# Kernel optimization log

Measured on AMD Instinct MI355X. Metric: run time of the kernel, lower is better.

The kernel has to match this reference:

```python
import jax, jax.numpy as jnp
import numpy as np

B, L, D, H = 2, 2048, 2048, 16
DH = D // H
ROPE_BASE = 10000.0


def _rope_cos_sin(seq_len, d_head, dtype=jnp.float32):
    # half-split RoPE: frequencies over even indices, repeated for both halves
    inv_freq = 1.0 / (ROPE_BASE ** (jnp.arange(0, d_head, 2, dtype=jnp.float32) / d_head))
    freqs = jnp.arange(seq_len, dtype=jnp.float32)[:, None] * inv_freq[None, :]  # [L, DH/2]
    emb = jnp.concatenate([freqs, freqs], axis=-1)  # [L, DH]
    return jnp.cos(emb).astype(dtype), jnp.sin(emb).astype(dtype)


def _rotate_half(x):
    x1, x2 = jnp.split(x, 2, axis=-1)
    return jnp.concatenate([-x2, x1], axis=-1)


def _apply_rope(x, cos, sin):
    # x: [B, H, L, DH]; cos/sin: [L, DH]
    return x * cos[None, None, :, :] + _rotate_half(x) * sin[None, None, :, :]


def setup_inputs() -> dict:
    key = jax.random.key(0)
    k1, k2, k3 = jax.random.split(key, 3)
    x = jax.random.normal(k1, (B, L, D), dtype=jnp.float32)
    w_qkv = jax.random.normal(k2, (3 * D, D), dtype=jnp.float32) * 0.02
    w_out = jax.random.normal(k3, (D, D), dtype=jnp.float32) * 0.02
    return {"x": x, "w_qkv": w_qkv, "w_out": w_out}


def reference(x, w_qkv, w_out):
    b, l, d = x.shape
    dh = d // H
    qkv = jnp.einsum('bld,ed->ble', x, w_qkv)  # [B, L, 3D]
    qkv = qkv.reshape(b, l, 3, H, dh)
    q = jnp.transpose(qkv[:, :, 0], (0, 2, 1, 3))  # [B, H, L, DH]
    k = jnp.transpose(qkv[:, :, 1], (0, 2, 1, 3))
    v = jnp.transpose(qkv[:, :, 2], (0, 2, 1, 3))
    cos, sin = _rope_cos_sin(l, dh, x.dtype)
    q = _apply_rope(q, cos, sin)
    k = _apply_rope(k, cos, sin)
    scale = 1.0 / jnp.sqrt(jnp.asarray(dh, dtype=x.dtype))
    scores = jnp.einsum('bhqd,bhkd->bhqk', q, k) * scale  # [B, H, L, L]
    causal = jnp.tril(jnp.ones((l, l), dtype=bool))
    scores = jnp.where(causal[None, None], scores, jnp.asarray(-jnp.inf, dtype=scores.dtype))
    attn = jax.nn.softmax(scores, axis=-1)
    out = jnp.einsum('bhqk,bhkd->bhqd', attn, v)  # [B, H, L, DH]
    out = jnp.transpose(out, (0, 2, 1, 3)).reshape(b, l, d)
    return jnp.einsum('bld,ed->ble', out, w_out)
```

## Files before the change

kernel.cpp:

```cpp
#include <hip/hip_runtime.h>
#include <hip/hip_bf16.h>

#define B_  2
#define L_  2048
#define D_  2048
#define H_  16
#define DH_ 128

typedef __attribute__((ext_vector_type(8))) short bf16x8;
typedef __attribute__((ext_vector_type(4))) short short4v;
typedef __attribute__((ext_vector_type(4))) float f32x4;
typedef __attribute__((ext_vector_type(16))) float f32x16;

__device__ __forceinline__ short f2bf(float f) {
  unsigned u = __float_as_uint(f);
  u = u + 0x7fffu + ((u >> 16) & 1u);
  return (short)(u >> 16);
}
__device__ __forceinline__ float bf2f(short s) {
  return __uint_as_float(((unsigned)(unsigned short)s) << 16);
}
__device__ __forceinline__ int pkbf(float a, float b) {
  return (int)(unsigned short)f2bf(a) | (((int)(unsigned short)f2bf(b)) << 16);
}

__global__ __launch_bounds__(256) void cvt_bf16_kernel(
    const float* __restrict__ in, short* __restrict__ out, int n4) {
  int i = blockIdx.x * 256 + threadIdx.x;
  if (i >= n4) return;
  float4 v = ((const float4*)in)[i];
  short4v o;
  o[0] = f2bf(v.x); o[1] = f2bf(v.y); o[2] = f2bf(v.z); o[3] = f2bf(v.w);
  ((short4v*)out)[i] = o;
}

__global__ __launch_bounds__(256) void rope_table_kernel(
    float* __restrict__ cost, float* __restrict__ sint) {
  int idx = blockIdx.x * 256 + threadIdx.x;
  int l = idx >> 6, j = idx & 63;
  float inv = powf(10000.0f, -(float)(2 * j) * (1.0f / 128.0f));
  float ang = (float)l * inv;
  cost[idx] = cosf(ang);
  sint[idx] = sinf(ang);
}

template<bool BF16OUT>
__global__ __launch_bounds__(256) void gemm_bt_kernel(
    const short* __restrict__ A, const short* __restrict__ Bm,
    void* __restrict__ Cv, int M, int N, int K) {
  __shared__ short As[128 * 32];
  __shared__ short Bs[128 * 32];
  const int tm = blockIdx.x * 128;
  const int tn = blockIdx.y * 128;
  const int tid = threadIdx.x;
  const int w = tid >> 6, l = tid & 63;
  const int wm = (w >> 1) * 64, wn = (w & 1) * 64;
  const int lr = l & 15, lk = (l >> 4) * 8;

  f32x4 acc[4][4] = {};

  for (int k0 = 0; k0 < K; k0 += 32) {
#pragma unroll
    for (int c = 0; c < 2; ++c) {
      int chunk = w * 2 + c;
      int elem = chunk * 512 + l * 8;
      int row = elem >> 5, col = elem & 31;
      __builtin_amdgcn_global_load_lds(
          (const __attribute__((address_space(1))) void*)(A + (size_t)(tm + row) * K + k0 + col),
          (__attribute__((address_space(3))) void*)(As + chunk * 512), 16, 0, 0);
      __builtin_amdgcn_global_load_lds(
          (const __attribute__((address_space(1))) void*)(Bm + (size_t)(tn + row) * K + k0 + col),
          (__attribute__((address_space(3))) void*)(Bs + chunk * 512), 16, 0, 0);
    }
    __syncthreads();
    bf16x8 af[4], bfr[4];
#pragma unroll
    for (int i = 0; i < 4; ++i) af[i]  = *(const bf16x8*)&As[(wm + i * 16 + lr) * 32 + lk];
#pragma unroll
    for (int j = 0; j < 4; ++j) bfr[j] = *(const bf16x8*)&Bs[(wn + j * 16 + lr) * 32 + lk];
#pragma unroll
    for (int i = 0; i < 4; ++i)
#pragma unroll
      for (int j = 0; j < 4; ++j)
        acc[i][j] = __builtin_amdgcn_mfma_f32_16x16x32_bf16(af[i], bfr[j], acc[i][j], 0, 0, 0);
    __syncthreads();
  }

  const int r0 = (l >> 4) * 4;
#pragma unroll
  for (int i = 0; i < 4; ++i)
#pragma unroll
    for (int j = 0; j < 4; ++j)
#pragma unroll
      for (int r = 0; r < 4; ++r) {
        size_t idx = (size_t)(tm + wm + i * 16 + r0 + r) * N + (tn + wn + j * 16 + lr);
        if (BF16OUT) ((short*)Cv)[idx] = f2bf(acc[i][j][r]);
        else         ((float*)Cv)[idx] = acc[i][j][r];
      }
}

__global__ __launch_bounds__(256) void rope_pack_kernel(
    const short* __restrict__ qkv, const float* __restrict__ cost,
    const float* __restrict__ sint, short* __restrict__ Qp,
    short* __restrict__ Kp) {
  int idx = blockIdx.x * 256 + threadIdx.x;
  int dh = idx & 63;
  int h  = (idx >> 6) & 15;
  int l  = (idx >> 10) & 2047;
  int b  = idx >> 21;
  size_t src = (size_t)(b * L_ + l) * (3 * D_);
  int e = h * DH_ + dh;
  float c = cost[l * 64 + dh], s = sint[l * 64 + dh];
  float q1 = bf2f(qkv[src + e]),        q2 = bf2f(qkv[src + e + 64]);
  float k1 = bf2f(qkv[src + D_ + e]),   k2 = bf2f(qkv[src + D_ + e + 64]);
  const float scale = 0.08838834764831845f;
  size_t dst = ((size_t)(b * H_ + h) * L_ + l) * DH_ + dh;
  Qp[dst]      = f2bf((q1 * c - q2 * s) * scale);
  Qp[dst + 64] = f2bf((q2 * c + q1 * s) * scale);
  Kp[dst]      = f2bf(k1 * c - k2 * s);
  Kp[dst + 64] = f2bf(k2 * c + k1 * s);
}

__global__ __launch_bounds__(256) void transpose_v_kernel(
    const short* __restrict__ qkv, short* __restrict__ VtG) {
  __shared__ short T[64 * 64];
  int bid = blockIdx.x;
  int lt = bid & 31, dt = (bid >> 5) & 1, bh = bid >> 6;
  int b = bh >> 4, h = bh & 15;
  int l0 = lt * 64, d0 = dt * 64;
  int tid = threadIdx.x;
#pragma unroll
  for (int it = 0; it < 2; ++it) {
    int row = it * 32 + (tid >> 3);
    int c   = (tid & 7) * 8;
    bf16x8 v = *(const bf16x8*)&qkv[(size_t)(b * L_ + l0 + row) * (3 * D_) + 2 * D_ + h * DH_ + d0 + c];
#pragma unroll
    for (int jj = 0; jj < 8; ++jj)
      T[row * 64 + ((c + jj + row) & 63)] = v[jj];
  }
  __syncthreads();
  int d = tid >> 2, lc = (tid & 3) * 16;
  short tmp[16];
#pragma unroll
  for (int j = 0; j < 16; ++j)
    tmp[j] = T[(lc + j) * 64 + ((d + lc + j) & 63)];
  size_t obase = (size_t)(bh * DH_ + d0 + d) * L_ + l0 + lc;
  *(bf16x8*)&VtG[obase]     = *(bf16x8*)&tmp[0];
  *(bf16x8*)&VtG[obase + 8] = *(bf16x8*)&tmp[8];
}

__global__ __launch_bounds__(256) void attn_kernel(
    const short* __restrict__ Qp, const short* __restrict__ Kp,
    const short* __restrict__ VtG, short* __restrict__ Out) {
  __shared__ short lds[2][16384];

  const int f   = blockIdx.x;
  const int bh  = (f & 7) + 8 * (f >> 7);
  const int qt  = (f >> 3) & 15;
  const int q0  = qt * 128;
  const int tid = threadIdx.x;
  const int w = tid >> 6, l = tid & 63;
  const int lq = l & 31, hi = l >> 5;
  const int qw = q0 + w * 32;
  const int b = bh >> 4, h = bh & 15;
  const size_t kqbase = (size_t)bh * (L_ * DH_);

  bf16x8 qf[8];
#pragma unroll
  for (int st = 0; st < 8; ++st)
    qf[st] = *(const bf16x8*)&Qp[kqbase + (size_t)(qw + lq) * DH_ + st * 16 + hi * 8];

  f32x16 oacc[4];
#pragma unroll
  for (int dm = 0; dm < 4; ++dm)
#pragma unroll
    for (int r = 0; r < 16; ++r) oacc[dm][r] = 0.f;
  float m_run = -1e30f, l_run = 0.f;

  const int nt = qt * 2 + 2;

  auto stage = [&](int bf, int kt) {
    int k0 = kt * 64;
#pragma unroll
    for (int i = 0; i < 4; ++i) {
      int c = w * 4 + i;
      int X = c * 1024 + l * 16;
      {
        int row = X >> 8, bcol = (X & 255) ^ ((row & 7) << 4);
        __builtin_amdgcn_global_load_lds(
            (const __attribute__((address_space(1))) void*)(Kp + kqbase + (size_t)(k0 + row) * DH_ + (bcol >> 1)),
            (__attribute__((address_space(3))) void*)(&lds[bf][c * 512]), 16, 0, 0);
      }
      {
        int row = X >> 7, bcol = (X & 127) ^ ((row & 7) << 4);
        __builtin_amdgcn_global_load_lds(
            (const __attribute__((address_space(1))) void*)(VtG + (size_t)(bh * DH_ + row) * L_ + k0 + (bcol >> 1)),
            (__attribute__((address_space(3))) void*)(&lds[bf][8192 + c * 512]), 16, 0, 0);
      }
    }
  };

  auto compute = [&](int bf, int kt) {
    int k0 = kt * 64;
    if (k0 > qw + 31) return;
    const char* ksB = (const char*)&lds[bf][0];
    const char* vsB = (const char*)&lds[bf][8192];

    f32x16 sacc[2];
#pragma unroll
    for (int fm = 0; fm < 2; ++fm)
#pragma unroll
      for (int r = 0; r < 16; ++r) sacc[fm][r] = 0.f;
#pragma unroll
    for (int st = 0; st < 8; ++st) {
#pragma unroll
      for (int fm = 0; fm < 2; ++fm) {
        int krow = fm * 32 + lq;
        int byte = (krow << 8) + ((st * 32 + hi * 16) ^ ((krow & 7) << 4));
        bf16x8 kf = *(const bf16x8*)(ksB + byte);
        sacc[fm] = __builtin_amdgcn_mfma_f32_32x32x16_bf16(kf, qf[st], sacc[fm], 0, 0, 0);
      }
    }

    if (k0 + 63 > qw) {
      int q = qw + lq;
#pragma unroll
      for (int fm = 0; fm < 2; ++fm)
#pragma unroll
        for (int r = 0; r < 16; ++r) {
          int k = k0 + fm * 32 + (r & 3) + 8 * (r >> 2) + 4 * hi;
          if (k > q) sacc[fm][r] = -1e30f;
        }
    }

    float pmax = sacc[0][0];
#pragma unroll
    for (int fm = 0; fm < 2; ++fm)
#pragma unroll
      for (int r = 0; r < 16; ++r) pmax = fmaxf(pmax, sacc[fm][r]);
    pmax = fmaxf(pmax, __shfl_xor(pmax, 32));
    float mnew = fmaxf(m_run, pmax);
    float alpha = __expf(m_run - mnew);
    m_run = mnew;
    float rsum = 0.f;
#pragma unroll
    for (int fm = 0; fm < 2; ++fm)
#pragma unroll
      for (int r = 0; r < 16; ++r) {
        float e = __expf(sacc[fm][r] - mnew);
        sacc[fm][r] = e;
        rsum += e;
      }
    rsum += __shfl_xor(rsum, 32);
    l_run = l_run * alpha + rsum;
#pragma unroll
    for (int dm = 0; dm < 4; ++dm)
#pragma unroll
      for (int r = 0; r < 16; ++r) oacc[dm][r] *= alpha;

    int pb[16];
#pragma unroll
    for (int fm = 0; fm < 2; ++fm)
#pragma unroll
      for (int i2 = 0; i2 < 8; ++i2)
        pb[fm * 8 + i2] = pkbf(sacc[fm][2 * i2], sacc[fm][2 * i2 + 1]);

#pragma unroll
    for (int kk = 0; kk < 4; ++kk) {
      int idx0 = (kk >> 1) * 8 + (kk & 1) * 4;
      int sw0 = __shfl_xor(pb[idx0],     32);
      int sw1 = __shfl_xor(pb[idx0 + 1], 32);
      int sw2 = __shfl_xor(pb[idx0 + 2], 32);
      int sw3 = __shfl_xor(pb[idx0 + 3], 32);
      union { int i[4]; bf16x8 v; } u;
      u.i[0] = hi ? sw2 : pb[idx0];
      u.i[1] = hi ? sw3 : pb[idx0 + 1];
      u.i[2] = hi ? pb[idx0 + 2] : sw0;
      u.i[3] = hi ? pb[idx0 + 3] : sw1;
#pragma unroll
      for (int dm = 0; dm < 4; ++dm) {
        int vrow = dm * 32 + lq;
        int byte = (vrow << 7) + ((kk * 32 + hi * 16) ^ ((vrow & 7) << 4));
        bf16x8 vf = *(const bf16x8*)(vsB + byte);
        oacc[dm] = __builtin_amdgcn_mfma_f32_32x32x16_bf16(vf, u.v, oacc[dm], 0, 0, 0);
      }
    }
  };

  stage(0, 0);
  __syncthreads();
  for (int kt = 0; kt < nt; ++kt) {
    if (kt + 1 < nt) stage((kt + 1) & 1, kt + 1);
    compute(kt & 1, kt);
    __syncthreads();
  }

  float inv = 1.0f / l_run;
  int q = qw + lq;
  size_t rowbase = ((size_t)(b * L_ + q)) * D_ + h * DH_;
#pragma unroll
  for (int dm = 0; dm < 4; ++dm)
#pragma unroll
    for (int g = 0; g < 4; ++g) {
      short4v s4;
#pragma unroll
      for (int t = 0; t < 4; ++t) s4[t] = f2bf(oacc[dm][4 * g + t] * inv);
      *(short4v*)&Out[rowbase + dm * 32 + 8 * g + 4 * hi] = s4;
    }
}

extern "C" void kernel_launch(void* const* d_in, const int* in_sizes, int n_in,
                              void* d_out, int out_size, void* d_ws, size_t ws_size,
                              hipStream_t stream) {
  const float* x     = (const float*)d_in[0];
  const float* w_qkv = (const float*)d_in[1];
  const float* w_out = (const float*)d_in[2];
  float* out = (float*)d_out;

  char* ws = (char*)d_ws;
  size_t off = 0;
  auto alloc = [&](size_t bytes) -> char* {
    char* p = ws + off;
    off += (bytes + 255) & ~(size_t)255;
    return p;
  };
  const size_t nX = (size_t)B_ * L_ * D_;
  const size_t nWqkv = (size_t)3 * D_ * D_;
  const size_t nWout = (size_t)D_ * D_;
  short* xb    = (short*)alloc(nX * 2);
  short* wqkvb = (short*)alloc(nWqkv * 2);
  short* woutb = (short*)alloc(nWout * 2);
  short* qkvb  = (short*)alloc((size_t)B_ * L_ * 3 * D_ * 2);
  short* Qp    = (short*)alloc(nX * 2);
  short* Kp    = (short*)alloc(nX * 2);
  short* VtG   = (short*)alloc(nX * 2);
  short* attnb = (short*)alloc(nX * 2);
  float* cost  = (float*)alloc((size_t)L_ * 64 * 4);
  float* sint  = (float*)alloc((size_t)L_ * 64 * 4);

  cvt_bf16_kernel<<<(int)(nX / 1024), 256, 0, stream>>>(x, xb, (int)(nX / 4));
  cvt_bf16_kernel<<<(int)(nWqkv / 1024), 256, 0, stream>>>(w_qkv, wqkvb, (int)(nWqkv / 4));
  cvt_bf16_kernel<<<(int)(nWout / 1024), 256, 0, stream>>>(w_out, woutb, (int)(nWout / 4));
  rope_table_kernel<<<(L_ * 64) / 256, 256, 0, stream>>>(cost, sint);
  gemm_bt_kernel<true><<<dim3(32, 48), 256, 0, stream>>>(xb, wqkvb, (void*)qkvb,
                                                         B_ * L_, 3 * D_, D_);
  rope_pack_kernel<<<(int)(nX / 512), 256, 0, stream>>>(qkvb, cost, sint, Qp, Kp);
  transpose_v_kernel<<<2048, 256, 0, stream>>>(qkvb, VtG);
  attn_kernel<<<512, 256, 0, stream>>>(Qp, Kp, VtG, attnb);
  gemm_bt_kernel<false><<<dim3(32, 16), 256, 0, stream>>>(attnb, woutb, (void*)out,
                                                          B_ * L_, D_, D_);
}
```

Before: 448.5 us.

## Rewrite GEMM with 256x128 tiles, triple-buffered LDS, swizzle and block remap

Replaces the 128x128 single-buffered GEMM with a 512-thread kernel computing 256x128 tiles over K-steps of 64. Global-to-LDS loads run through a three-stage ring buffer, prefetching two tiles ahead and waiting with explicit vmcnt counts, so memory latency overlaps the MFMA work. LDS rows use an XOR swizzle to avoid bank conflicts, and block IDs are remapped for better L2 locality. MFMA sections are wrapped in raised wave priority. The costs are 144KB of LDS per block, which limits occupancy, and more fragile hand-written synchronisation.

New measurement: 395.9 us. -11.7%, faster.

```diff
diff --git a/kernel.cpp b/kernel.cpp
--- a/kernel.cpp
+++ b/kernel.cpp
@@ -45,57 +45,128 @@
 }
 
 template<bool BF16OUT>
-__global__ __launch_bounds__(256) void gemm_bt_kernel(
+__global__ __launch_bounds__(512, 2) void gemm256_kernel(
     const short* __restrict__ A, const short* __restrict__ Bm,
-    void* __restrict__ Cv, int M, int N, int K) {
-  __shared__ short As[128 * 32];
-  __shared__ short Bs[128 * 32];
-  const int tm = blockIdx.x * 128;
-  const int tn = blockIdx.y * 128;
+    void* __restrict__ Cv, int M, int N, int K, int nbn) {
+  __shared__ short lds[3][24576];
+  const int NT = K >> 6;
   const int tid = threadIdx.x;
   const int w = tid >> 6, l = tid & 63;
-  const int wm = (w >> 1) * 64, wn = (w & 1) * 64;
-  const int lr = l & 15, lk = (l >> 4) * 8;
+  const int wrm = w >> 1, wnn = w & 1;
+  const int lr = l & 15, c4 = l >> 4;
+
+  const int cpx = gridDim.x >> 3;
+  const int bid = blockIdx.x;
+  const int swz = (bid & 7) * cpx + (bid >> 3);
+  const int bm = swz / nbn, bn = swz % nbn;
+  const int tm = bm * 256, tn = bn * 128;
+
+  const char* srcA[4];
+  const char* srcB[2];
+#pragma unroll
+  for (int s = 0; s < 4; ++s) {
+    int X = (s * 512 + tid) * 16;
+    int row = X >> 7;
+    int koff = (X & 127) ^ ((row & 7) << 4);
+    srcA[s] = (const char*)A + ((size_t)(tm + row) * K) * 2 + koff;
+  }
+#pragma unroll
+  for (int s = 0; s < 2; ++s) {
+    int X = (s * 512 + tid) * 16;
+    int row = X >> 7;
+    int koff = (X & 127) ^ ((row & 7) << 4);
+    srcB[s] = (const char*)Bm + ((size_t)(tn + row) * K) * 2 + koff;
+  }
+
+  int offA[4][2], offB[4][2];
+#pragma unroll
+  for (int m = 0; m < 4; ++m) {
+    int row = wrm * 64 + m * 16 + lr;
+#pragma unroll
+    for (int kk = 0; kk < 2; ++kk)
+      offA[m][kk] = row * 128 + ((kk * 64 + c4 * 16) ^ ((row & 7) << 4));
+  }
+#pragma unroll
+  for (int n = 0; n < 4; ++n) {
+    int row = wnn * 64 + n * 16 + lr;
+#pragma unroll
+    for (int kk = 0; kk < 2; ++kk)
+      offB[n][kk] = row * 128 + ((kk * 64 + c4 * 16) ^ ((row & 7) << 4));
+  }
+
+  auto issueA = [&](int jj, int buf) {
+#pragma unroll
+    for (int s = 0; s < 4; ++s)
+      __builtin_amdgcn_global_load_lds(
+          (const __attribute__((address_space(1))) void*)(srcA[s] + (size_t)jj * 128),
+          (__attribute__((address_space(3))) void*)(&lds[buf][s * 4096 + w * 512]),
+          16, 0, 0);
+  };
+  auto issueB = [&](int jj, int buf) {
+#pragma unroll
+    for (int s = 0; s < 2; ++s)
+      __builtin_amdgcn_global_load_lds(
+          (const __attribute__((address_space(1))) void*)(srcB[s] + (size_t)jj * 128),
+          (__attribute__((address_space(3))) void*)(&lds[buf][16384 + s * 4096 + w * 512]),
+          16, 0, 0);
+  };
 
   f32x4 acc[4][4] = {};
 
-  for (int k0 = 0; k0 < K; k0 += 32) {
-#pragma unroll
-    for (int c = 0; c < 2; ++c) {
-      int chunk = w * 2 + c;
-      int elem = chunk * 512 + l * 8;
-      int row = elem >> 5, col = elem & 31;
-      __builtin_amdgcn_global_load_lds(
-          (const __attribute__((address_space(1))) void*)(A + (size_t)(tm + row) * K + k0 + col),
-          (__attribute__((address_space(3))) void*)(As + chunk * 512), 16, 0, 0);
-      __builtin_amdgcn_global_load_lds(
-          (const __attribute__((address_space(1))) void*)(Bm + (size_t)(tn + row) * K + k0 + col),
-          (__attribute__((address_space(3))) void*)(Bs + chunk * 512), 16, 0, 0);
-    }
-    __syncthreads();
-    bf16x8 af[4], bfr[4];
-#pragma unroll
-    for (int i = 0; i < 4; ++i) af[i]  = *(const bf16x8*)&As[(wm + i * 16 + lr) * 32 + lk];
-#pragma unroll
-    for (int j = 0; j < 4; ++j) bfr[j] = *(const bf16x8*)&Bs[(wn + j * 16 + lr) * 32 + lk];
-#pragma unroll
-    for (int i = 0; i < 4; ++i)
-#pragma unroll
-      for (int j = 0; j < 4; ++j)
-        acc[i][j] = __builtin_amdgcn_mfma_f32_16x16x32_bf16(af[i], bfr[j], acc[i][j], 0, 0, 0);
-    __syncthreads();
-  }
-
-  const int r0 = (l >> 4) * 4;
-#pragma unroll
-  for (int i = 0; i < 4; ++i)
-#pragma unroll
-    for (int j = 0; j < 4; ++j)
+  issueA(0, 0); issueB(0, 0);
+  if (NT > 1) { issueA(1, 1); issueB(1, 1); }
+
+  int cur = 0;
+  for (int j = 0; j < NT; ++j) {
+    if (j == NT - 1) asm volatile("s_waitcnt vmcnt(0)" ::: "memory");
+    else             asm volatile("s_waitcnt vmcnt(6)" ::: "memory");
+    __builtin_amdgcn_s_barrier();
+    int pf = cur + 2; if (pf >= 3) pf -= 3;
+    const char* aB = (const char*)&lds[cur][0];
+    const char* bB = (const char*)&lds[cur][16384];
+
+    if (j + 2 < NT) issueA(j + 2, pf);
+    bf16x8 af[4], bfv[4];
+#pragma unroll
+    for (int m = 0; m < 4; ++m) af[m]  = *(const bf16x8*)(aB + offA[m][0]);
+#pragma unroll
+    for (int n = 0; n < 4; ++n) bfv[n] = *(const bf16x8*)(bB + offB[n][0]);
+    __builtin_amdgcn_s_barrier();
+    __builtin_amdgcn_s_setprio(1);
+#pragma unroll
+    for (int m = 0; m < 4; ++m)
+#pragma unroll
+      for (int n = 0; n < 4; ++n)
+        acc[m][n] = __builtin_amdgcn_mfma_f32_16x16x32_bf16(af[m], bfv[n], acc[m][n], 0, 0, 0);
+    __builtin_amdgcn_s_setprio(0);
+
+    if (j + 2 < NT) issueB(j + 2, pf);
+#pragma unroll
+    for (int m = 0; m < 4; ++m) af[m]  = *(const bf16x8*)(aB + offA[m][1]);
+#pragma unroll
+    for (int n = 0; n < 4; ++n) bfv[n] = *(const bf16x8*)(bB + offB[n][1]);
+    __builtin_amdgcn_s_barrier();
+    __builtin_amdgcn_s_setprio(1);
+#pragma unroll
+    for (int m = 0; m < 4; ++m)
+#pragma unroll
+      for (int n = 0; n < 4; ++n)
+        acc[m][n] = __builtin_amdgcn_mfma_f32_16x16x32_bf16(af[m], bfv[n], acc[m][n], 0, 0, 0);
+    __builtin_amdgcn_s_setprio(0);
+
+    cur = cur + 1; if (cur >= 3) cur = 0;
+  }
+
+#pragma unroll
+  for (int m = 0; m < 4; ++m)
+#pragma unroll
+    for (int n = 0; n < 4; ++n)
 #pragma unroll
       for (int r = 0; r < 4; ++r) {
-        size_t idx = (size_t)(tm + wm + i * 16 + r0 + r) * N + (tn + wn + j * 16 + lr);
-        if (BF16OUT) ((short*)Cv)[idx] = f2bf(acc[i][j][r]);
-        else         ((float*)Cv)[idx] = acc[i][j][r];
+        size_t idx = (size_t)(tm + wrm * 64 + m * 16 + c4 * 4 + r) * N
+                   + (tn + wnn * 64 + n * 16 + lr);
+        if (BF16OUT) ((short*)Cv)[idx] = f2bf(acc[m][n][r]);
+        else         ((float*)Cv)[idx] = acc[m][n][r];
       }
 }
 
@@ -342,11 +413,11 @@
   cvt_bf16_kernel<<<(int)(nWqkv / 1024), 256, 0, stream>>>(w_qkv, wqkvb, (int)(nWqkv / 4));
   cvt_bf16_kernel<<<(int)(nWout / 1024), 256, 0, stream>>>(w_out, woutb, (int)(nWout / 4));
   rope_table_kernel<<<(L_ * 64) / 256, 256, 0, stream>>>(cost, sint);
-  gemm_bt_kernel<true><<<dim3(32, 48), 256, 0, stream>>>(xb, wqkvb, (void*)qkvb,
-                                                         B_ * L_, 3 * D_, D_);
+  gemm256_kernel<true><<<768, 512, 0, stream>>>(xb, wqkvb, (void*)qkvb,
+                                                B_ * L_, 3 * D_, D_, 48);
   rope_pack_kernel<<<(int)(nX / 512), 256, 0, stream>>>(qkvb, cost, sint, Qp, Kp);
   transpose_v_kernel<<<2048, 256, 0, stream>>>(qkvb, VtG);
   attn_kernel<<<512, 256, 0, stream>>>(Qp, Kp, VtG, attnb);
-  gemm_bt_kernel<false><<<dim3(32, 16), 256, 0, stream>>>(attnb, woutb, (void*)out,
-                                                          B_ * L_, D_, D_);
-}
+  gemm256_kernel<false><<<256, 512, 0, stream>>>(attnb, woutb, (void*)out,
+                                                 B_ * L_, D_, D_, 16);
+}
```
